# Kernel optimization log

Hardware: AMD Instinct MI355X
Metric: run time of the kernel (lower is better)

The kernel has to match this reference:

```python
import jax, jax.numpy as jnp
from jax import lax
import numpy as np
import math

DIM = 96      # channels
HEADS = 3     # num_heads
WS = 8        # window size
SHIFT = 4     # window_size // 2 (depth is odd -> shifted)
TLC = 64      # tlc_kernel
H = 264
W = 264


def _grid_idxes(h, w, k1, k2):
    # Faithful replication of the torch grids() tiling index logic (static ints).
    num_row = (h - 1) // k1 + 1
    num_col = (w - 1) // k2 + 1
    step_j = k2 if num_col == 1 else math.ceil((w - k2) / (num_col - 1) - 1e-8)
    step_i = k1 if num_row == 1 else math.ceil((h - k1) / (num_row - 1) - 1e-8)
    idxes = []
    i = 0
    last_i = False
    while i < h and not last_i:
        j = 0
        if i + k1 >= h:
            i = h - k1
            last_i = True
        last_j = False
        while j < w and not last_j:
            if j + k2 >= w:
                j = w - k2
                last_j = True
            idxes.append((i, j))
            j = j + step_j
        i = i + step_i
    return idxes


def setup_inputs() -> dict:
    key = jax.random.key(0)
    ks = jax.random.split(key, 4)
    return {
        "x": jax.random.normal(ks[0], (1, DIM, H, W), jnp.float32),
        "temperature": jnp.ones((HEADS, 1, 1), jnp.float32),
        "qkv_w": jax.random.normal(ks[1], (3 * DIM, DIM), jnp.float32) * 0.05,
        "dw_w": jax.random.normal(ks[2], (3 * DIM, 1, 3, 3), jnp.float32) * 0.1,
        "proj_w": jax.random.normal(ks[3], (DIM, DIM), jnp.float32) * 0.05,
    }


def reference(x, temperature, qkv_w, dw_w, proj_w):
    b, c, h, w = x.shape
    # depth % 2 == 1 -> cyclic shift
    x = jnp.roll(x, (-SHIFT, -SHIFT), axis=(2, 3))
    # 1x1 pointwise conv (no bias)
    qkv = jnp.einsum('oc,bchw->bohw', qkv_w, x)
    # 3x3 depthwise conv, padding 1
    qkv = lax.conv_general_dilated(
        qkv, dw_w, window_strides=(1, 1), padding=[(1, 1), (1, 1)],
        feature_group_count=3 * c, dimension_numbers=('NCHW', 'OIHW', 'NCHW'))
    # --- TLC grids: overlapping tiles (eval path, b == 1) ---
    k1, k2 = min(h, TLC), min(w, TLC)
    idxes = _grid_idxes(h, w, k1, k2)
    parts = jnp.concatenate([qkv[:, :, i:i + k1, j:j + k2] for (i, j) in idxes], axis=0)  # [T,3c,k1,k2]
    T, C3, th, tw = parts.shape
    nh, nw = th // WS, tw // WS
    # window partition: b c (h b0) (w b1) -> (b h w) c b0 b1 -> flatten spatial
    win = parts.reshape(T, C3, nh, WS, nw, WS).transpose(0, 2, 4, 1, 3, 5)
    win = win.reshape(T * nh * nw, C3, WS * WS)  # [Bw, 3c, 64]
    q, k, v = jnp.split(win, 3, axis=1)  # each [Bw, c, 64]
    ch = c // HEADS
    q = q.reshape(-1, HEADS, ch, WS * WS)
    k = k.reshape(-1, HEADS, ch, WS * WS)
    v = v.reshape(-1, HEADS, ch, WS * WS)
    # L2 normalize along token dim (F.normalize eps=1e-12)
    q = q / jnp.maximum(jnp.linalg.norm(q, axis=-1, keepdims=True), 1e-12)
    k = k / jnp.maximum(jnp.linalg.norm(k, axis=-1, keepdims=True), 1e-12)
    # channel attention: [Bw, head, ch, ch]
    attn = jax.nn.relu(jnp.einsum('bhcn,bhdn->bhcd', q, k) * temperature)
    out = jnp.einsum('bhcd,bhdn->bhcn', attn, v)  # [Bw, head, ch, 64]
    out = out.reshape(-1, c, WS, WS)
    # window merge back to tiles
    out = out.reshape(T, nh, nw, c, WS, WS).transpose(0, 3, 1, 4, 2, 5).reshape(T, c, th, tw)
    # --- TLC grids_inverse: scatter-add overlapping tiles and average ---
    preds = jnp.zeros((b, c, h, w), x.dtype)
    cnt = np.zeros((h, w), np.float32)
    for t, (i, j) in enumerate(idxes):
        preds = preds.at[0, :, i:i + k1, j:j + k2].add(out[t])
        cnt[i:i + k1, j:j + k2] += 1.0
    preds = preds / jnp.asarray(cnt)
    # 1x1 output projection
    out = jnp.einsum('oc,bchw->bohw', proj_w, preds)
    # undo cyclic shift
    return jnp.roll(out, (SHIFT, SHIFT), axis=(2, 3))
```

## Files before the change

kernel.cpp:

```cpp
#include <hip/hip_runtime.h>
#include <hip/hip_bf16.h>

#define HW_ 69696
#define W_ 264
#define H_ 264

typedef short bf16x8 __attribute__((ext_vector_type(8)));
typedef float f32x4 __attribute__((ext_vector_type(4)));

static __device__ __forceinline__ unsigned short f2b(float f) {
  __hip_bfloat16 h = __float2bfloat16(f);
  return *reinterpret_cast<unsigned short*>(&h);
}
static __device__ __forceinline__ float b2f(unsigned short u) {
  __hip_bfloat16 h;
  *reinterpret_cast<unsigned short*>(&h) = u;
  return __bfloat162float(h);
}
static __device__ __forceinline__ float lo_f(unsigned int u) {
  union { unsigned int i; float f; } c; c.i = u << 16; return c.f;
}
static __device__ __forceinline__ float hi_f(unsigned int u) {
  union { unsigned int i; float f; } c; c.i = u & 0xffff0000u; return c.f;
}

__global__ __launch_bounds__(256, 4) void k_gemm(const float* __restrict__ x,
                                                 const float* __restrict__ w,
                                                 unsigned short* __restrict__ outb) {
  __shared__ __align__(16) char smem[19968];
  unsigned short* As = (unsigned short*)smem;
  unsigned short* Cs = (unsigned short*)smem;

  const int tid = threadIdx.x;
  const int wid = tid >> 6, lane = tid & 63;
  const int quad = lane >> 4, lo = lane & 15;
  const int px0 = blockIdx.x * 64;
  const int px = px0 + wid * 16 + lo;

  const int y = px / W_, xx = px - y * W_;
  int y2 = y + 4; if (y2 >= H_) y2 -= H_;
  int x2 = xx + 4; if (x2 >= W_) x2 -= W_;
  const float* xb = x + y2 * W_ + x2;

  bf16x8 bf[3];
#pragma unroll
  for (int ks = 0; ks < 3; ++ks) {
    const float* xp = xb + (size_t)(ks * 32 + quad * 8) * HW_;
    float f[8];
#pragma unroll
    for (int i = 0; i < 8; ++i) f[i] = xp[(size_t)i * HW_];
    union { bf16x8 v; unsigned short s[8]; } u;
#pragma unroll
    for (int i = 0; i < 8; ++i) u.s[i] = f2b(f[i]);
    bf[ks] = u.v;
  }

  for (int oc = 0; oc < 3; ++oc) {
    __syncthreads();
    const float* wp = w + oc * 96 * 96;
    for (int l = tid; l < 96 * 24; l += 256) {
      int o = l / 24, c4 = (l - (l / 24) * 24) * 4;
      float4 v = *(const float4*)&wp[o * 96 + c4];
      unsigned int p0 = (unsigned int)f2b(v.x) | ((unsigned int)f2b(v.y) << 16);
      unsigned int p1 = (unsigned int)f2b(v.z) | ((unsigned int)f2b(v.w) << 16);
      *(uint2*)&As[o * 104 + c4] = make_uint2(p0, p1);
    }
    __syncthreads();

    f32x4 acc[6];
#pragma unroll
    for (int mt = 0; mt < 6; ++mt) acc[mt] = {0.f, 0.f, 0.f, 0.f};
#pragma unroll
    for (int ks = 0; ks < 3; ++ks) {
      const int kb = ks * 32 + quad * 8;
#pragma unroll
      for (int mt = 0; mt < 6; ++mt) {
        bf16x8 a = *(const bf16x8*)&As[(mt * 16 + lo) * 104 + kb];
        acc[mt] = __builtin_amdgcn_mfma_f32_16x16x32_bf16(a, bf[ks], acc[mt], 0, 0, 0);
      }
    }
    __syncthreads();

    const int pxl = wid * 16 + lo;
#pragma unroll
    for (int mt = 0; mt < 6; ++mt) {
      unsigned int p0 = (unsigned int)f2b(acc[mt][0]) | ((unsigned int)f2b(acc[mt][1]) << 16);
      unsigned int p1 = (unsigned int)f2b(acc[mt][2]) | ((unsigned int)f2b(acc[mt][3]) << 16);
      *(uint2*)&Cs[pxl * 104 + mt * 16 + quad * 4] = make_uint2(p0, p1);
    }
    __syncthreads();

    for (int i = tid; i < 64 * 12; i += 256) {
      int pxl2 = i & 63, j = i >> 6;
      *((uint4*)outb + (size_t)(oc * 12 + j) * HW_ + px0 + pxl2) =
          ((const uint4*)(Cs + pxl2 * 104))[j];
    }
  }
}

__global__ __launch_bounds__(256, 3) void k_dwattn(const unsigned short* __restrict__ qkvb,
                                                   const float* __restrict__ dwv,
                                                   const float* __restrict__ temp,
                                                   unsigned short* __restrict__ tout) {
  __shared__ __align__(16) unsigned short outS[64 * 296];
  __shared__ __align__(16) uint4 stg[4][100];
  __shared__ __align__(16) unsigned short attnL[3 * 32 * 40];
  __shared__ float invn[3 * 32];

  const int tid = threadIdx.x;
  const int wi = ((blockIdx.x & 7) << 3) | (blockIdx.x >> 3);
  const int t = blockIdx.y;
  const int i0 = (t / 5) * 50, j0 = (t % 5) * 50;
  const int wy = wi >> 3, wx = wi & 7;
  const int gy0 = i0 + wy * 8, gx0 = j0 + wx * 8;

  const int h = tid >> 6, lane = tid & 63;
  const int w_ = __builtin_amdgcn_readfirstlane(h);

  {
    uint4* stgW = &stg[w_][0];
    const int r0 = lane >> 3, c0 = lane & 7;
    const int sy0 = lane / 10, sx0 = lane - sy0 * 10;
    const int ii1 = lane + 64;
    const int sy1 = ii1 / 10, sx1 = ii1 - sy1 * 10;
    const int gyA = gy0 - 1 + sy0, gxA = gx0 - 1 + sx0;
    const int gyB = gy0 - 1 + sy1, gxB = gx0 - 1 + sx1;
    const bool okA = (unsigned)gyA < (unsigned)H_ && (unsigned)gxA < (unsigned)W_;
    const bool okB = ii1 < 100 && (unsigned)gyB < (unsigned)H_ && (unsigned)gxB < (unsigned)W_;
    const size_t offA = (size_t)gyA * W_ + gxA;
    const size_t offB = (size_t)gyB * W_ + gxB;
    const uint4* qb4 = (const uint4*)qkvb;

    uint4 vA = okA ? qb4[(size_t)w_ * HW_ + offA] : make_uint4(0u, 0u, 0u, 0u);
    uint4 vB = okB ? qb4[(size_t)w_ * HW_ + offB] : make_uint4(0u, 0u, 0u, 0u);

    for (int k = 0; k < 9; ++k) {
      const int u = k * 4 + w_;
      stgW[lane] = vA;
      if (ii1 < 100) stgW[ii1] = vB;
      if (k < 8) {
        vA = okA ? qb4[(size_t)(u + 4) * HW_ + offA] : make_uint4(0u, 0u, 0u, 0u);
        vB = okB ? qb4[(size_t)(u + 4) * HW_ + offB] : make_uint4(0u, 0u, 0u, 0u);
      }
      asm volatile("s_waitcnt lgkmcnt(0)" ::: "memory");
      __builtin_amdgcn_sched_barrier(0);

      const float* wp = dwv + u * 72;
      float acc[8] = {0.f, 0.f, 0.f, 0.f, 0.f, 0.f, 0.f, 0.f};
#pragma unroll
      for (int dy = 0; dy < 3; ++dy)
#pragma unroll
        for (int dx = 0; dx < 3; ++dx) {
          uint4 v = stgW[(r0 + dy) * 10 + (c0 + dx)];
          float w0 = wp[0 * 9 + dy * 3 + dx], w1 = wp[1 * 9 + dy * 3 + dx];
          float w2 = wp[2 * 9 + dy * 3 + dx], w3 = wp[3 * 9 + dy * 3 + dx];
          float w4 = wp[4 * 9 + dy * 3 + dx], w5 = wp[5 * 9 + dy * 3 + dx];
          float w6 = wp[6 * 9 + dy * 3 + dx], w7 = wp[7 * 9 + dy * 3 + dx];
          acc[0] += w0 * lo_f(v.x); acc[1] += w1 * hi_f(v.x);
          acc[2] += w2 * lo_f(v.y); acc[3] += w3 * hi_f(v.y);
          acc[4] += w4 * lo_f(v.z); acc[5] += w5 * hi_f(v.z);
          acc[6] += w6 * lo_f(v.w); acc[7] += w7 * hi_f(v.w);
        }
      uint4 o;
      o.x = (unsigned int)f2b(acc[0]) | ((unsigned int)f2b(acc[1]) << 16);
      o.y = (unsigned int)f2b(acc[2]) | ((unsigned int)f2b(acc[3]) << 16);
      o.z = (unsigned int)f2b(acc[4]) | ((unsigned int)f2b(acc[5]) << 16);
      o.w = (unsigned int)f2b(acc[6]) | ((unsigned int)f2b(acc[7]) << 16);
      *(uint4*)&outS[lane * 296 + u * 8] = o;
    }
  }
  __syncthreads();

  const int quad = lane >> 4, lo = lane & 15;
  const int cb = h * 32;

  bf16x8 qf[2][2], kf[2][2];
  f32x4 S[2][2];
  float ivk[2];
  if (h < 3) {
#pragma unroll
    for (int mt = 0; mt < 2; ++mt)
#pragma unroll
      for (int kt = 0; kt < 2; ++kt) {
        const int rr = kt * 4 + quad;
        const int cq = cb + mt * 16 + lo;
        const int ck = 96 + cq;
        bf16x8 q8, k8;
#pragma unroll
        for (int j = 0; j < 8; ++j) {
          q8[j] = (short)outS[(rr * 8 + j) * 296 + cq];
          k8[j] = (short)outS[(rr * 8 + j) * 296 + ck];
        }
        qf[mt][kt] = q8;
        kf[mt][kt] = k8;
      }

#pragma unroll
    for (int mt = 0; mt < 2; ++mt)
#pragma unroll
      for (int nt = 0; nt < 2; ++nt) {
        S[mt][nt] = {0.f, 0.f, 0.f, 0.f};
#pragma unroll
        for (int kt = 0; kt < 2; ++kt)
          S[mt][nt] = __builtin_amdgcn_mfma_f32_16x16x32_bf16(qf[mt][kt], kf[nt][kt], S[mt][nt], 0, 0, 0);
      }

#pragma unroll
    for (int mt = 0; mt < 2; ++mt) {
      float sq = 0.f, sk = 0.f;
#pragma unroll
      for (int kt = 0; kt < 2; ++kt)
#pragma unroll
        for (int j = 0; j < 8; ++j) {
          float a = b2f((unsigned short)qf[mt][kt][j]);
          float b = b2f((unsigned short)kf[mt][kt][j]);
          sq += a * a;
          sk += b * b;
        }
      sq += __shfl_xor(sq, 16);
      sq += __shfl_xor(sq, 32);
      sk += __shfl_xor(sk, 16);
      sk += __shfl_xor(sk, 32);
      if (quad == 0) invn[h * 32 + mt * 16 + lo] = 1.f / fmaxf(sqrtf(sq), 1e-12f);
      ivk[mt] = 1.f / fmaxf(sqrtf(sk), 1e-12f);
    }
  }
  __syncthreads();

  if (h < 3) {
    const float ts = temp[h];
#pragma unroll
    for (int mt = 0; mt < 2; ++mt)
#pragma unroll
      for (int nt = 0; nt < 2; ++nt)
#pragma unroll
        for (int r = 0; r < 4; ++r) {
          int c = mt * 16 + quad * 4 + r;
          float v = S[mt][nt][r] * invn[h * 32 + c] * ivk[nt] * ts;
          attnL[(h * 32 + c) * 40 + nt * 16 + lo] = f2b(fmaxf(v, 0.f));
        }
  }
  __syncthreads();

  f32x4 O[2][4];
  if (h < 3) {
    bf16x8 af[2];
#pragma unroll
    for (int mt = 0; mt < 2; ++mt)
      af[mt] = *(const bf16x8*)&attnL[(h * 32 + mt * 16 + lo) * 40 + quad * 8];

    const int uv = 24 + h * 4 + quad;
#pragma unroll
    for (int nt = 0; nt < 4; ++nt) {
      const int px = nt * 16 + lo;
      uint4 vraw = *(const uint4*)&outS[px * 296 + uv * 8];
      bf16x8 vf = *reinterpret_cast<bf16x8*>(&vraw);
#pragma unroll
      for (int mt = 0; mt < 2; ++mt) {
        f32x4 z = {0.f, 0.f, 0.f, 0.f};
        O[mt][nt] = __builtin_amdgcn_mfma_f32_16x16x32_bf16(af[mt], vf, z, 0, 0, 0);
      }
    }
  }
  __syncthreads();

  unsigned short* Cs = outS;
  if (h < 3) {
#pragma unroll
    for (int mt = 0; mt < 2; ++mt)
#pragma unroll
      for (int nt = 0; nt < 4; ++nt) {
        const int px = nt * 16 + lo;
        unsigned int p0 = (unsigned int)f2b(O[mt][nt][0]) | ((unsigned int)f2b(O[mt][nt][1]) << 16);
        unsigned int p1 = (unsigned int)f2b(O[mt][nt][2]) | ((unsigned int)f2b(O[mt][nt][3]) << 16);
        *(uint2*)&Cs[px * 104 + cb + mt * 16 + quad * 4] = make_uint2(p0, p1);
      }
  }
  __syncthreads();

  for (int idx = tid; idx < 64 * 12; idx += 256) {
    int u = idx >> 6, rec = idx & 63;
    int r = rec >> 3, j = rec & 7;
    size_t local = (size_t)(wy * 8 + r) * 64 + wx * 8 + j;
    ((uint4*)tout)[((size_t)t * 12 + u) * 4096 + local] = ((const uint4*)(Cs + rec * 104))[u];
  }
}

__global__ __launch_bounds__(256, 4) void k_avgproj(const float* __restrict__ w,
                                                    const unsigned short* __restrict__ tout,
                                                    float* __restrict__ outf) {
  __shared__ __align__(16) unsigned short As[96 * 104];
  const int tid = threadIdx.x;
  const int wid = tid >> 6, lane = tid & 63;
  const int quad = lane >> 4, lo = lane & 15;
  const int px0 = blockIdx.x * 64;
  const int px = px0 + wid * 16 + lo;

  for (int l = tid; l < 96 * 24; l += 256) {
    int o = l / 24, c4 = (l - (l / 24) * 24) * 4;
    float4 v = *(const float4*)&w[o * 96 + c4];
    unsigned int p0 = (unsigned int)f2b(v.x) | ((unsigned int)f2b(v.y) << 16);
    unsigned int p1 = (unsigned int)f2b(v.z) | ((unsigned int)f2b(v.w) << 16);
    *(uint2*)&As[o * 104 + c4] = make_uint2(p0, p1);
  }

  const int y = px / W_, xx = px - y * W_;
  int loy = (y >= 64) ? (y - 14) / 50 : 0;
  int hiy = y / 50; if (hiy > 4) hiy = 4;
  int lox = (xx >= 64) ? (xx - 14) / 50 : 0;
  int hix = xx / 50; if (hix > 4) hix = 4;
  float a24[24];
#pragma unroll
  for (int i = 0; i < 24; ++i) a24[i] = 0.f;
  int cnt = 0;
  for (int ty = loy; ty <= hiy; ++ty)
    for (int tx = lox; tx <= hix; ++tx) {
      size_t local = (size_t)((y - ty * 50) << 6) + (xx - tx * 50);
      const uint4* rp = (const uint4*)tout +
                        ((size_t)(ty * 5 + tx) * 12 + quad) * 4096 + local;
#pragma unroll
      for (int ks = 0; ks < 3; ++ks) {
        uint4 v = rp[(size_t)ks * 4 * 4096];
        a24[ks * 8 + 0] += lo_f(v.x); a24[ks * 8 + 1] += hi_f(v.x);
        a24[ks * 8 + 2] += lo_f(v.y); a24[ks * 8 + 3] += hi_f(v.y);
        a24[ks * 8 + 4] += lo_f(v.z); a24[ks * 8 + 5] += hi_f(v.z);
        a24[ks * 8 + 6] += lo_f(v.w); a24[ks * 8 + 7] += hi_f(v.w);
      }
      ++cnt;
    }
  const float inv = 1.f / (float)cnt;
  bf16x8 bf[3];
#pragma unroll
  for (int ks = 0; ks < 3; ++ks) {
    union { bf16x8 v; unsigned short s[8]; } u;
#pragma unroll
    for (int i = 0; i < 8; ++i) u.s[i] = f2b(a24[ks * 8 + i] * inv);
    bf[ks] = u.v;
  }
  __syncthreads();

  f32x4 acc[6];
#pragma unroll
  for (int mt = 0; mt < 6; ++mt) acc[mt] = {0.f, 0.f, 0.f, 0.f};
#pragma unroll
  for (int ks = 0; ks < 3; ++ks) {
    const int kb = ks * 32 + quad * 8;
#pragma unroll
    for (int mt = 0; mt < 6; ++mt) {
      bf16x8 a = *(const bf16x8*)&As[(mt * 16 + lo) * 104 + kb];
      acc[mt] = __builtin_amdgcn_mfma_f32_16x16x32_bf16(a, bf[ks], acc[mt], 0, 0, 0);
    }
  }

  {
    int y2 = y + 4; if (y2 >= H_) y2 -= H_;
    int x2 = xx + 4; if (x2 >= W_) x2 -= W_;
    int tp = y2 * W_ + x2;
#pragma unroll
    for (int mt = 0; mt < 6; ++mt) {
      int row = mt * 16 + quad * 4;
#pragma unroll
      for (int r = 0; r < 4; ++r)
        outf[(size_t)(row + r) * HW_ + tp] = acc[mt][r];
    }
  }
}

extern "C" void kernel_launch(void* const* d_in, const int* in_sizes, int n_in,
                              void* d_out, int out_size, void* d_ws, size_t ws_size,
                              hipStream_t stream) {
  (void)in_sizes; (void)n_in; (void)out_size; (void)ws_size;
  const float* x = (const float*)d_in[0];
  const float* temp = (const float*)d_in[1];
  const float* qkvw = (const float*)d_in[2];
  const float* dww = (const float*)d_in[3];
  const float* projw = (const float*)d_in[4];
  float* out = (float*)d_out;

  char* ws = (char*)d_ws;
  const size_t SZQ = (size_t)288 * HW_ * 2;
  unsigned short* qkvb = (unsigned short*)ws;
  unsigned short* tout = (unsigned short*)(ws + SZQ);

  k_gemm<<<dim3(1089), 256, 0, stream>>>(x, qkvw, qkvb);
  k_dwattn<<<dim3(64, 25), 256, 0, stream>>>(qkvb, dww, temp, tout);
  k_avgproj<<<dim3(1089), 256, 0, stream>>>(projw, tout, out);
}
```

Before: 141.7 us.

## Write GEMM output directly from registers, process two windows per attention block

The QKV GEMM kernel no longer stages its result through shared memory. Each lane writes its 8-byte bf16 pieces straight to global memory, which drops two barriers and the LDS round trip at the cost of narrower, less coalesced stores. The depthwise+attention kernel now loops over two adjacent windows per block and launches half as many blocks, which amortises launch overhead but serialises work inside each block. Occupancy hints on the GEMM and projection kernels are raised from 4 to 5 blocks per CU.

```diff
diff --git a/kernel.cpp b/kernel.cpp
--- a/kernel.cpp
+++ b/kernel.cpp
@@ -24,12 +24,10 @@
   union { unsigned int i; float f; } c; c.i = u & 0xffff0000u; return c.f;
 }
 
-__global__ __launch_bounds__(256, 4) void k_gemm(const float* __restrict__ x,
+__global__ __launch_bounds__(256, 5) void k_gemm(const float* __restrict__ x,
                                                  const float* __restrict__ w,
                                                  unsigned short* __restrict__ outb) {
-  __shared__ __align__(16) char smem[19968];
-  unsigned short* As = (unsigned short*)smem;
-  unsigned short* Cs = (unsigned short*)smem;
+  __shared__ __align__(16) unsigned short As[96 * 104];
 
   const int tid = threadIdx.x;
   const int wid = tid >> 6, lane = tid & 63;
@@ -42,7 +40,7 @@
   int x2 = xx + 4; if (x2 >= W_) x2 -= W_;
   const float* xb = x + y2 * W_ + x2;
 
-  bf16x8 bf[3];
+  bf16x8 bfv[3];
 #pragma unroll
   for (int ks = 0; ks < 3; ++ks) {
     const float* xp = xb + (size_t)(ks * 32 + quad * 8) * HW_;
@@ -52,7 +50,7 @@
     union { bf16x8 v; unsigned short s[8]; } u;
 #pragma unroll
     for (int i = 0; i < 8; ++i) u.s[i] = f2b(f[i]);
-    bf[ks] = u.v;
+    bfv[ks] = u.v;
   }
 
   for (int oc = 0; oc < 3; ++oc) {
@@ -76,24 +74,16 @@
 #pragma unroll
       for (int mt = 0; mt < 6; ++mt) {
         bf16x8 a = *(const bf16x8*)&As[(mt * 16 + lo) * 104 + kb];
-        acc[mt] = __builtin_amdgcn_mfma_f32_16x16x32_bf16(a, bf[ks], acc[mt], 0, 0, 0);
-      }
-    }
-    __syncthreads();
-
-    const int pxl = wid * 16 + lo;
+        acc[mt] = __builtin_amdgcn_mfma_f32_16x16x32_bf16(a, bfv[ks], acc[mt], 0, 0, 0);
+      }
+    }
+
 #pragma unroll
     for (int mt = 0; mt < 6; ++mt) {
+      const int u = oc * 12 + 2 * mt + (quad >> 1);
       unsigned int p0 = (unsigned int)f2b(acc[mt][0]) | ((unsigned int)f2b(acc[mt][1]) << 16);
       unsigned int p1 = (unsigned int)f2b(acc[mt][2]) | ((unsigned int)f2b(acc[mt][3]) << 16);
-      *(uint2*)&Cs[pxl * 104 + mt * 16 + quad * 4] = make_uint2(p0, p1);
-    }
-    __syncthreads();
-
-    for (int i = tid; i < 64 * 12; i += 256) {
-      int pxl2 = i & 63, j = i >> 6;
-      *((uint4*)outb + (size_t)(oc * 12 + j) * HW_ + px0 + pxl2) =
-          ((const uint4*)(Cs + pxl2 * 104))[j];
+      *(uint2*)((char*)outb + ((size_t)u * HW_ + px) * 16 + (quad & 1) * 8) = make_uint2(p0, p1);
     }
   }
 }
@@ -108,185 +98,191 @@
   __shared__ float invn[3 * 32];
 
   const int tid = threadIdx.x;
-  const int wi = ((blockIdx.x & 7) << 3) | (blockIdx.x >> 3);
+  const int bx = blockIdx.x;
+  const int pair = ((bx & 7) << 2) | (bx >> 3);
   const int t = blockIdx.y;
   const int i0 = (t / 5) * 50, j0 = (t % 5) * 50;
-  const int wy = wi >> 3, wx = wi & 7;
-  const int gy0 = i0 + wy * 8, gx0 = j0 + wx * 8;
+  const int wy = pair >> 2, wx0 = (pair & 3) * 2;
 
   const int h = tid >> 6, lane = tid & 63;
   const int w_ = __builtin_amdgcn_readfirstlane(h);
-
-  {
-    uint4* stgW = &stg[w_][0];
-    const int r0 = lane >> 3, c0 = lane & 7;
-    const int sy0 = lane / 10, sx0 = lane - sy0 * 10;
-    const int ii1 = lane + 64;
-    const int sy1 = ii1 / 10, sx1 = ii1 - sy1 * 10;
-    const int gyA = gy0 - 1 + sy0, gxA = gx0 - 1 + sx0;
-    const int gyB = gy0 - 1 + sy1, gxB = gx0 - 1 + sx1;
-    const bool okA = (unsigned)gyA < (unsigned)H_ && (unsigned)gxA < (unsigned)W_;
-    const bool okB = ii1 < 100 && (unsigned)gyB < (unsigned)H_ && (unsigned)gxB < (unsigned)W_;
-    const size_t offA = (size_t)gyA * W_ + gxA;
-    const size_t offB = (size_t)gyB * W_ + gxB;
-    const uint4* qb4 = (const uint4*)qkvb;
-
-    uint4 vA = okA ? qb4[(size_t)w_ * HW_ + offA] : make_uint4(0u, 0u, 0u, 0u);
-    uint4 vB = okB ? qb4[(size_t)w_ * HW_ + offB] : make_uint4(0u, 0u, 0u, 0u);
-
-    for (int k = 0; k < 9; ++k) {
-      const int u = k * 4 + w_;
-      stgW[lane] = vA;
-      if (ii1 < 100) stgW[ii1] = vB;
-      if (k < 8) {
-        vA = okA ? qb4[(size_t)(u + 4) * HW_ + offA] : make_uint4(0u, 0u, 0u, 0u);
-        vB = okB ? qb4[(size_t)(u + 4) * HW_ + offB] : make_uint4(0u, 0u, 0u, 0u);
-      }
-      asm volatile("s_waitcnt lgkmcnt(0)" ::: "memory");
-      __builtin_amdgcn_sched_barrier(0);
-
-      const float* wp = dwv + u * 72;
-      float acc[8] = {0.f, 0.f, 0.f, 0.f, 0.f, 0.f, 0.f, 0.f};
-#pragma unroll
-      for (int dy = 0; dy < 3; ++dy)
-#pragma unroll
-        for (int dx = 0; dx < 3; ++dx) {
-          uint4 v = stgW[(r0 + dy) * 10 + (c0 + dx)];
-          float w0 = wp[0 * 9 + dy * 3 + dx], w1 = wp[1 * 9 + dy * 3 + dx];
-          float w2 = wp[2 * 9 + dy * 3 + dx], w3 = wp[3 * 9 + dy * 3 + dx];
-          float w4 = wp[4 * 9 + dy * 3 + dx], w5 = wp[5 * 9 + dy * 3 + dx];
-          float w6 = wp[6 * 9 + dy * 3 + dx], w7 = wp[7 * 9 + dy * 3 + dx];
-          acc[0] += w0 * lo_f(v.x); acc[1] += w1 * hi_f(v.x);
-          acc[2] += w2 * lo_f(v.y); acc[3] += w3 * hi_f(v.y);
-          acc[4] += w4 * lo_f(v.z); acc[5] += w5 * hi_f(v.z);
-          acc[6] += w6 * lo_f(v.w); acc[7] += w7 * hi_f(v.w);
-        }
-      uint4 o;
-      o.x = (unsigned int)f2b(acc[0]) | ((unsigned int)f2b(acc[1]) << 16);
-      o.y = (unsigned int)f2b(acc[2]) | ((unsigned int)f2b(acc[3]) << 16);
-      o.z = (unsigned int)f2b(acc[4]) | ((unsigned int)f2b(acc[5]) << 16);
-      o.w = (unsigned int)f2b(acc[6]) | ((unsigned int)f2b(acc[7]) << 16);
-      *(uint4*)&outS[lane * 296 + u * 8] = o;
-    }
-  }
-  __syncthreads();
-
   const int quad = lane >> 4, lo = lane & 15;
-  const int cb = h * 32;
-
-  bf16x8 qf[2][2], kf[2][2];
-  f32x4 S[2][2];
-  float ivk[2];
-  if (h < 3) {
-#pragma unroll
-    for (int mt = 0; mt < 2; ++mt)
-#pragma unroll
-      for (int kt = 0; kt < 2; ++kt) {
-        const int rr = kt * 4 + quad;
-        const int cq = cb + mt * 16 + lo;
-        const int ck = 96 + cq;
-        bf16x8 q8, k8;
-#pragma unroll
-        for (int j = 0; j < 8; ++j) {
-          q8[j] = (short)outS[(rr * 8 + j) * 296 + cq];
-          k8[j] = (short)outS[(rr * 8 + j) * 296 + ck];
-        }
-        qf[mt][kt] = q8;
-        kf[mt][kt] = k8;
-      }
-
-#pragma unroll
-    for (int mt = 0; mt < 2; ++mt)
-#pragma unroll
-      for (int nt = 0; nt < 2; ++nt) {
-        S[mt][nt] = {0.f, 0.f, 0.f, 0.f};
+
+  uint4* stgW = &stg[w_][0];
+  const int r0 = lane >> 3, c0 = lane & 7;
+  const int sy0 = lane / 10, sx0 = lane - sy0 * 10;
+  const int ii1 = lane + 64;
+  const int sy1 = ii1 / 10, sx1 = ii1 - sy1 * 10;
+  const uint4* qb4 = (const uint4*)qkvb;
+
+  for (int w2 = 0; w2 < 2; ++w2) {
+    const int wx = wx0 + w2;
+    const int gy0 = i0 + wy * 8, gx0 = j0 + wx * 8;
+
+    {
+      const int gyA = gy0 - 1 + sy0, gxA = gx0 - 1 + sx0;
+      const int gyB = gy0 - 1 + sy1, gxB = gx0 - 1 + sx1;
+      const bool okA = (unsigned)gyA < (unsigned)H_ && (unsigned)gxA < (unsigned)W_;
+      const bool okB = ii1 < 100 && (unsigned)gyB < (unsigned)H_ && (unsigned)gxB < (unsigned)W_;
+      const size_t offA = (size_t)gyA * W_ + gxA;
+      const size_t offB = (size_t)gyB * W_ + gxB;
+
+      uint4 vA = okA ? qb4[(size_t)w_ * HW_ + offA] : make_uint4(0u, 0u, 0u, 0u);
+      uint4 vB = okB ? qb4[(size_t)w_ * HW_ + offB] : make_uint4(0u, 0u, 0u, 0u);
+
+      for (int k = 0; k < 9; ++k) {
+        const int u = k * 4 + w_;
+        stgW[lane] = vA;
+        if (ii1 < 100) stgW[ii1] = vB;
+        if (k < 8) {
+          vA = okA ? qb4[(size_t)(u + 4) * HW_ + offA] : make_uint4(0u, 0u, 0u, 0u);
+          vB = okB ? qb4[(size_t)(u + 4) * HW_ + offB] : make_uint4(0u, 0u, 0u, 0u);
+        }
+        asm volatile("s_waitcnt lgkmcnt(0)" ::: "memory");
+        __builtin_amdgcn_sched_barrier(0);
+
+        const float* wp = dwv + u * 72;
+        float acc[8] = {0.f, 0.f, 0.f, 0.f, 0.f, 0.f, 0.f, 0.f};
+#pragma unroll
+        for (int dy = 0; dy < 3; ++dy)
+#pragma unroll
+          for (int dx = 0; dx < 3; ++dx) {
+            uint4 v = stgW[(r0 + dy) * 10 + (c0 + dx)];
+            float w0 = wp[0 * 9 + dy * 3 + dx], w1 = wp[1 * 9 + dy * 3 + dx];
+            float w2v = wp[2 * 9 + dy * 3 + dx], w3 = wp[3 * 9 + dy * 3 + dx];
+            float w4 = wp[4 * 9 + dy * 3 + dx], w5 = wp[5 * 9 + dy * 3 + dx];
+            float w6 = wp[6 * 9 + dy * 3 + dx], w7 = wp[7 * 9 + dy * 3 + dx];
+            acc[0] += w0 * lo_f(v.x); acc[1] += w1 * hi_f(v.x);
+            acc[2] += w2v * lo_f(v.y); acc[3] += w3 * hi_f(v.y);
+            acc[4] += w4 * lo_f(v.z); acc[5] += w5 * hi_f(v.z);
+            acc[6] += w6 * lo_f(v.w); acc[7] += w7 * hi_f(v.w);
+          }
+        uint4 o;
+        o.x = (unsigned int)f2b(acc[0]) | ((unsigned int)f2b(acc[1]) << 16);
+        o.y = (unsigned int)f2b(acc[2]) | ((unsigned int)f2b(acc[3]) << 16);
+        o.z = (unsigned int)f2b(acc[4]) | ((unsigned int)f2b(acc[5]) << 16);
+        o.w = (unsigned int)f2b(acc[6]) | ((unsigned int)f2b(acc[7]) << 16);
+        *(uint4*)&outS[lane * 296 + u * 8] = o;
+      }
+    }
+    __syncthreads();
+
+    const int cb = h * 32;
+    f32x4 S[2][2];
+    bf16x8 qf[2][2], kf[2][2];
+    float ivk[2];
+    if (h < 3) {
+#pragma unroll
+      for (int mt = 0; mt < 2; ++mt)
+#pragma unroll
+        for (int kt = 0; kt < 2; ++kt) {
+          const int rr = kt * 4 + quad;
+          const int cq = cb + mt * 16 + lo;
+          const int ck = 96 + cq;
+          bf16x8 q8, k8;
+#pragma unroll
+          for (int j = 0; j < 8; ++j) {
+            q8[j] = (short)outS[(rr * 8 + j) * 296 + cq];
+            k8[j] = (short)outS[(rr * 8 + j) * 296 + ck];
+          }
+          qf[mt][kt] = q8;
+          kf[mt][kt] = k8;
+        }
+
+#pragma unroll
+      for (int mt = 0; mt < 2; ++mt)
+#pragma unroll
+        for (int nt = 0; nt < 2; ++nt) {
+          S[mt][nt] = {0.f, 0.f, 0.f, 0.f};
+#pragma unroll
+          for (int kt = 0; kt < 2; ++kt)
+            S[mt][nt] = __builtin_amdgcn_mfma_f32_16x16x32_bf16(qf[mt][kt], kf[nt][kt], S[mt][nt], 0, 0, 0);
+        }
+
+#pragma unroll
+      for (int mt = 0; mt < 2; ++mt) {
+        float sq = 0.f, sk = 0.f;
 #pragma unroll
         for (int kt = 0; kt < 2; ++kt)
-          S[mt][nt] = __builtin_amdgcn_mfma_f32_16x16x32_bf16(qf[mt][kt], kf[nt][kt], S[mt][nt], 0, 0, 0);
-      }
-
-#pragma unroll
-    for (int mt = 0; mt < 2; ++mt) {
-      float sq = 0.f, sk = 0.f;
-#pragma unroll
-      for (int kt = 0; kt < 2; ++kt)
-#pragma unroll
-        for (int j = 0; j < 8; ++j) {
-          float a = b2f((unsigned short)qf[mt][kt][j]);
-          float b = b2f((unsigned short)kf[mt][kt][j]);
-          sq += a * a;
-          sk += b * b;
-        }
-      sq += __shfl_xor(sq, 16);
-      sq += __shfl_xor(sq, 32);
-      sk += __shfl_xor(sk, 16);
-      sk += __shfl_xor(sk, 32);
-      if (quad == 0) invn[h * 32 + mt * 16 + lo] = 1.f / fmaxf(sqrtf(sq), 1e-12f);
-      ivk[mt] = 1.f / fmaxf(sqrtf(sk), 1e-12f);
-    }
-  }
-  __syncthreads();
-
-  if (h < 3) {
-    const float ts = temp[h];
-#pragma unroll
-    for (int mt = 0; mt < 2; ++mt)
-#pragma unroll
-      for (int nt = 0; nt < 2; ++nt)
-#pragma unroll
-        for (int r = 0; r < 4; ++r) {
-          int c = mt * 16 + quad * 4 + r;
-          float v = S[mt][nt][r] * invn[h * 32 + c] * ivk[nt] * ts;
-          attnL[(h * 32 + c) * 40 + nt * 16 + lo] = f2b(fmaxf(v, 0.f));
-        }
-  }
-  __syncthreads();
-
-  f32x4 O[2][4];
-  if (h < 3) {
-    bf16x8 af[2];
-#pragma unroll
-    for (int mt = 0; mt < 2; ++mt)
-      af[mt] = *(const bf16x8*)&attnL[(h * 32 + mt * 16 + lo) * 40 + quad * 8];
-
-    const int uv = 24 + h * 4 + quad;
-#pragma unroll
-    for (int nt = 0; nt < 4; ++nt) {
-      const int px = nt * 16 + lo;
-      uint4 vraw = *(const uint4*)&outS[px * 296 + uv * 8];
-      bf16x8 vf = *reinterpret_cast<bf16x8*>(&vraw);
-#pragma unroll
-      for (int mt = 0; mt < 2; ++mt) {
-        f32x4 z = {0.f, 0.f, 0.f, 0.f};
-        O[mt][nt] = __builtin_amdgcn_mfma_f32_16x16x32_bf16(af[mt], vf, z, 0, 0, 0);
-      }
-    }
-  }
-  __syncthreads();
-
-  unsigned short* Cs = outS;
-  if (h < 3) {
-#pragma unroll
-    for (int mt = 0; mt < 2; ++mt)
+#pragma unroll
+          for (int j = 0; j < 8; ++j) {
+            float a = b2f((unsigned short)qf[mt][kt][j]);
+            float b = b2f((unsigned short)kf[mt][kt][j]);
+            sq += a * a;
+            sk += b * b;
+          }
+        sq += __shfl_xor(sq, 16);
+        sq += __shfl_xor(sq, 32);
+        sk += __shfl_xor(sk, 16);
+        sk += __shfl_xor(sk, 32);
+        if (quad == 0) invn[h * 32 + mt * 16 + lo] = 1.f / fmaxf(sqrtf(sq), 1e-12f);
+        ivk[mt] = 1.f / fmaxf(sqrtf(sk), 1e-12f);
+      }
+    }
+    __syncthreads();
+
+    if (h < 3) {
+      const float ts = temp[h];
+#pragma unroll
+      for (int mt = 0; mt < 2; ++mt)
+#pragma unroll
+        for (int nt = 0; nt < 2; ++nt)
+#pragma unroll
+          for (int r = 0; r < 4; ++r) {
+            int c = mt * 16 + quad * 4 + r;
+            float v = S[mt][nt][r] * invn[h * 32 + c] * ivk[nt] * ts;
+            attnL[(h * 32 + c) * 40 + nt * 16 + lo] = f2b(fmaxf(v, 0.f));
+          }
+    }
+    __syncthreads();
+
+    f32x4 O[2][4];
+    if (h < 3) {
+      bf16x8 af[2];
+#pragma unroll
+      for (int mt = 0; mt < 2; ++mt)
+        af[mt] = *(const bf16x8*)&attnL[(h * 32 + mt * 16 + lo) * 40 + quad * 8];
+
+      const int uv = 24 + h * 4 + quad;
 #pragma unroll
       for (int nt = 0; nt < 4; ++nt) {
         const int px = nt * 16 + lo;
-        unsigned int p0 = (unsigned int)f2b(O[mt][nt][0]) | ((unsigned int)f2b(O[mt][nt][1]) << 16);
-        unsigned int p1 = (unsigned int)f2b(O[mt][nt][2]) | ((unsigned int)f2b(O[mt][nt][3]) << 16);
-        *(uint2*)&Cs[px * 104 + cb + mt * 16 + quad * 4] = make_uint2(p0, p1);
-      }
-  }
-  __syncthreads();
-
-  for (int idx = tid; idx < 64 * 12; idx += 256) {
-    int u = idx >> 6, rec = idx & 63;
-    int r = rec >> 3, j = rec & 7;
-    size_t local = (size_t)(wy * 8 + r) * 64 + wx * 8 + j;
-    ((uint4*)tout)[((size_t)t * 12 + u) * 4096 + local] = ((const uint4*)(Cs + rec * 104))[u];
-  }
-}
-
-__global__ __launch_bounds__(256, 4) void k_avgproj(const float* __restrict__ w,
+        uint4 vraw = *(const uint4*)&outS[px * 296 + uv * 8];
+        bf16x8 vf = *reinterpret_cast<bf16x8*>(&vraw);
+#pragma unroll
+        for (int mt = 0; mt < 2; ++mt) {
+          f32x4 z = {0.f, 0.f, 0.f, 0.f};
+          O[mt][nt] = __builtin_amdgcn_mfma_f32_16x16x32_bf16(af[mt], vf, z, 0, 0, 0);
+        }
+      }
+    }
+    __syncthreads();
+
+    unsigned short* Cs = outS;
+    if (h < 3) {
+#pragma unroll
+      for (int mt = 0; mt < 2; ++mt)
+#pragma unroll
+        for (int nt = 0; nt < 4; ++nt) {
+          const int px = nt * 16 + lo;
+          unsigned int p0 = (unsigned int)f2b(O[mt][nt][0]) | ((unsigned int)f2b(O[mt][nt][1]) << 16);
+          unsigned int p1 = (unsigned int)f2b(O[mt][nt][2]) | ((unsigned int)f2b(O[mt][nt][3]) << 16);
+          *(uint2*)&Cs[px * 104 + cb + mt * 16 + quad * 4] = make_uint2(p0, p1);
+        }
+    }
+    __syncthreads();
+
+    for (int idx = tid; idx < 64 * 12; idx += 256) {
+      int u = idx >> 6, rec = idx & 63;
+      int r = rec >> 3, j = rec & 7;
+      size_t local = (size_t)(wy * 8 + r) * 64 + wx * 8 + j;
+      ((uint4*)tout)[((size_t)t * 12 + u) * 4096 + local] = ((const uint4*)(Cs + rec * 104))[u];
+    }
+    __syncthreads();
+  }
+}
+
+__global__ __launch_bounds__(256, 5) void k_avgproj(const float* __restrict__ w,
                                                     const unsigned short* __restrict__ tout,
                                                     float* __restrict__ outf) {
   __shared__ __align__(16) unsigned short As[96 * 104];
@@ -329,13 +325,13 @@
       ++cnt;
     }
   const float inv = 1.f / (float)cnt;
-  bf16x8 bf[3];
+  bf16x8 bfv[3];
 #pragma unroll
   for (int ks = 0; ks < 3; ++ks) {
     union { bf16x8 v; unsigned short s[8]; } u;
 #pragma unroll
     for (int i = 0; i < 8; ++i) u.s[i] = f2b(a24[ks * 8 + i] * inv);
-    bf[ks] = u.v;
+    bfv[ks] = u.v;
   }
   __syncthreads();
 
@@ -348,7 +344,7 @@
 #pragma unroll
     for (int mt = 0; mt < 6; ++mt) {
       bf16x8 a = *(const bf16x8*)&As[(mt * 16 + lo) * 104 + kb];
-      acc[mt] = __builtin_amdgcn_mfma_f32_16x16x32_bf16(a, bf[ks], acc[mt], 0, 0, 0);
+      acc[mt] = __builtin_amdgcn_mfma_f32_16x16x32_bf16(a, bfv[ks], acc[mt], 0, 0, 0);
     }
   }
 
@@ -383,6 +379,6 @@
   unsigned short* tout = (unsigned short*)(ws + SZQ);
 
   k_gemm<<<dim3(1089), 256, 0, stream>>>(x, qkvw, qkvb);
-  k_dwattn<<<dim3(64, 25), 256, 0, stream>>>(qkvb, dww, temp, tout);
+  k_dwattn<<<dim3(32, 25), 256, 0, stream>>>(qkvb, dww, temp, tout);
   k_avgproj<<<dim3(1089), 256, 0, stream>>>(projw, tout, out);
 }
```

Result: slower. 150.2 us (+6.0%).
